# Kernel optimization log

Hardware: AMD Instinct MI355X
Metric: run time of the kernel (lower is better)

The kernel has to match this reference:

```python
import jax, jax.numpy as jnp
import numpy as np
import math

IN_FEATURES = 4096
OUT_FEATURES = 4096
N_ROWS = 8192
EPS = 1e-6
ROOT2 = math.sqrt(2.0)


def setup_inputs() -> dict:
    key = jax.random.key(0)
    k1, k2 = jax.random.split(key)
    # p_x: probabilities in [0,1]
    p_x = jax.random.uniform(k1, (N_ROWS, IN_FEATURES), dtype=jnp.float32)
    # weight ~ Uniform(-2, 2) per reset_parameters
    weight = jax.random.uniform(k2, (OUT_FEATURES, IN_FEATURES), dtype=jnp.float32, minval=-2.0, maxval=2.0)
    return {"p_x": p_x, "weight": weight}


def reference(p_x, weight):
    in_features = weight.shape[1]
    threshold = -(-in_features // 2)  # ceil(in_features / 2)
    p_w = jax.nn.sigmoid(weight)  # (O, I)
    # p_success = 2*p_w*p_x + 1 - p_x - p_w = c*p_x + d, with:
    c = 2.0 * p_w - 1.0          # (O, I)
    d = 1.0 - p_w                # (O, I)
    # mu = sum_i p_success = p_x @ c^T + sum_i d   -- never materialize (..., O, I)
    mu = jnp.einsum('ni,oi->no', p_x, c) + jnp.sum(d, axis=-1)  # (N, O)
    # sum_i p_success^2 = p_x^2 @ (c^2)^T + 2 * p_x @ (c*d)^T + sum_i d^2
    sum_sq = (jnp.einsum('ni,oi->no', p_x * p_x, c * c)
              + 2.0 * jnp.einsum('ni,oi->no', p_x, c * d)
              + jnp.sum(d * d, axis=-1))  # (N, O)
    # sum p_success*(1 - p_success) = mu - sum_sq
    sigma = jnp.sqrt(mu - sum_sq + EPS)  # (N, O)
    p_actives = 0.5 - 0.5 * jax.lax.erf((threshold - 0.5 - mu) / (sigma * ROOT2))
    return p_actives
```

## Files before the change

kernel.cpp:

```cpp
#include <hip/hip_runtime.h>
#include <hip/hip_bf16.h>
#include <math.h>
#include <cstdint>

#define KDIM 4096
#define ODIM 4096
#define MDIM 8192
#define EPSF 1e-6f
#define TM05 2047.5f

typedef __bf16 bf16x8 __attribute__((ext_vector_type(8)));
typedef float f32x4 __attribute__((ext_vector_type(4)));
typedef unsigned short u16;

#define XY_DELTA (MDIM * KDIM)
#define CD_DELTA (ODIM * KDIM)

#define NITER (KDIM / 128)

__device__ __forceinline__ u16 f2bf(float f) {
  __hip_bfloat16 h = __float2bfloat16(f);
  return __builtin_bit_cast(u16, h);
}
__device__ __forceinline__ float bf2f(u16 b) {
  unsigned int u = ((unsigned int)b) << 16;
  return __builtin_bit_cast(float, u);
}

__device__ __forceinline__ void async_cp16(void* lds, const void* g) {
  __builtin_amdgcn_global_load_lds(
      (__attribute__((address_space(1))) void*)(uintptr_t)g,
      (__attribute__((address_space(3))) void*)lds, 16, 0, 0);
}

__global__ void prep_x_kernel(const float4* __restrict__ x4,
                              ushort4* __restrict__ Xb,
                              ushort4* __restrict__ Yb) {
  int i = blockIdx.x * blockDim.x + threadIdx.x;
  float4 v = x4[i];
  ushort4 xo, yo;
  xo.x = f2bf(v.x); xo.y = f2bf(v.y); xo.z = f2bf(v.z); xo.w = f2bf(v.w);
  yo.x = f2bf(v.x * (1.0f - v.x));
  yo.y = f2bf(v.y * (1.0f - v.y));
  yo.z = f2bf(v.z * (1.0f - v.z));
  yo.w = f2bf(v.w * (1.0f - v.w));
  Xb[i] = xo;
  Yb[i] = yo;
}

__device__ __forceinline__ void wcomp(float w, u16& cb, u16& c2b, float& sd, float& sde) {
  float pw = 1.0f / (1.0f + __expf(-w));
  float c  = 2.0f * pw - 1.0f;
  float d  = 1.0f - pw;
  cb  = f2bf(c);
  c2b = f2bf(c * c);
  sd  += d;
  sde += d * pw;
}

__global__ void prep_w_kernel(const float4* __restrict__ w4,
                              ushort4* __restrict__ Cb,
                              ushort4* __restrict__ C2b,
                              float* __restrict__ sumd,
                              float* __restrict__ sumde) {
  const int o = blockIdx.x;
  const int t = threadIdx.x;
  const float4* wr = w4 + (size_t)o * (KDIM / 4);
  ushort4* cr  = Cb  + (size_t)o * (KDIM / 4);
  ushort4* c2r = C2b + (size_t)o * (KDIM / 4);
  float sd = 0.f, sde = 0.f;
#pragma unroll
  for (int it = 0; it < KDIM / 4 / 256; ++it) {
    int k4 = t + it * 256;
    float4 w = wr[k4];
    ushort4 co, c2o;
    wcomp(w.x, co.x, c2o.x, sd, sde);
    wcomp(w.y, co.y, c2o.y, sd, sde);
    wcomp(w.z, co.z, c2o.z, sd, sde);
    wcomp(w.w, co.w, c2o.w, sd, sde);
    cr[k4]  = co;
    c2r[k4] = c2o;
  }
#pragma unroll
  for (int off = 32; off > 0; off >>= 1) {
    sd  += __shfl_down(sd, off);
    sde += __shfl_down(sde, off);
  }
  __shared__ float red[8];
  if ((t & 63) == 0) { red[t >> 6] = sd; red[4 + (t >> 6)] = sde; }
  __syncthreads();
  if (t == 0) {
    sumd[o]  = red[0] + red[1] + red[2] + red[3];
    sumde[o] = red[4] + red[5] + red[6] + red[7];
  }
}


#define STG2(bb, isB, half, src, koff) do {                                    \
    char* _d = smem + (bb) * 65536 + (isB) * 32768 + (half) * 16384 + tid * 16;\
    const u16* _s = (src) + (size_t)((half) * 128) * KDIM + (koff);            \
    async_cp16(_d, _s);                                                        \
    async_cp16(_d + 8192, _s + (size_t)64 * KDIM);                             \
  } while (0)

#define BAR   asm volatile("s_barrier" ::: "memory")
#define BARV4 asm volatile("s_waitcnt vmcnt(4)\n\ts_barrier" ::: "memory")
#define BARV0 asm volatile("s_waitcnt vmcnt(0)\n\ts_barrier" ::: "memory")

#define PH(bb, AI, MO, GK, BARR, DOB, STG, ENDBAR) {                           \
    const char* Ab = smem + (bb) * 65536;                                      \
    const char* Bb = Ab + 32768;                                               \
    bf16x8 x0 = *(const bf16x8*)(Ab + arow + (MO) + 0 * 2048 + (GK));          \
    bf16x8 x1 = *(const bf16x8*)(Ab + arow + (MO) + 1 * 2048 + (GK));          \
    bf16x8 x2 = *(const bf16x8*)(Ab + arow + (MO) + 2 * 2048 + (GK));          \
    bf16x8 x3 = *(const bf16x8*)(Ab + arow + (MO) + 3 * 2048 + (GK));          \
    if (DOB) {                                                                 \
      _Pragma("unroll") for (int j = 0; j < 4; ++j)                            \
        BARR[j] = *(const bf16x8*)(Bb + brow + j * 2048 + (GK));               \
    }                                                                          \
    STG;                                                                       \
    asm volatile("s_waitcnt lgkmcnt(0)" ::: "memory");                         \
    __builtin_amdgcn_sched_barrier(0);                                         \
    __builtin_amdgcn_s_setprio(1);                                             \
    _Pragma("unroll") for (int j = 0; j < 4; ++j)                              \
      acc[(AI) + 0][j] = __builtin_amdgcn_mfma_f32_16x16x32_bf16(x0, BARR[j], acc[(AI) + 0][j], 0, 0, 0); \
    _Pragma("unroll") for (int j = 0; j < 4; ++j)                              \
      acc[(AI) + 1][j] = __builtin_amdgcn_mfma_f32_16x16x32_bf16(x1, BARR[j], acc[(AI) + 1][j], 0, 0, 0); \
    _Pragma("unroll") for (int j = 0; j < 4; ++j)                              \
      acc[(AI) + 2][j] = __builtin_amdgcn_mfma_f32_16x16x32_bf16(x2, BARR[j], acc[(AI) + 2][j], 0, 0, 0); \
    _Pragma("unroll") for (int j = 0; j < 4; ++j)                              \
      acc[(AI) + 3][j] = __builtin_amdgcn_mfma_f32_16x16x32_bf16(x3, BARR[j], acc[(AI) + 3][j], 0, 0, 0); \
    __builtin_amdgcn_s_setprio(0);                                             \
    ENDBAR;                                                                    \
  }

template <int PASS>
__global__ __launch_bounds__(512, 2) void gemm_pass_kernel(
    const u16* __restrict__ Ag, const u16* __restrict__ Bg,
    const float* __restrict__ sumd, const float* __restrict__ sumde,
    float* __restrict__ out) {
  __shared__ __attribute__((aligned(128))) char smem[2 * 65536];

  const int tid  = threadIdx.x;
  const int lane = tid & 63;
  const int wave = tid >> 6;
  const int wr   = wave >> 2;
  const int wc   = wave & 3;
  const int quad = lane >> 4;
  const int r16  = lane & 15;

  const int raw = blockIdx.x;
  const int wg  = (raw & 7) * 64 + (raw >> 3);
  const int n0  = (wg >> 5) * 256;
  const int m0  = (wg & 31) * 256;

  const int srow = tid >> 3;
  const int scol = ((tid & 7) ^ (srow & 7)) * 8;
  const u16* gA = Ag + (size_t)(m0 + srow) * KDIM + scol;
  const u16* gB = Bg + (size_t)(n0 + srow) * KDIM + scol;

  const int r7   = r16 & 7;
  const int g0   = (quad ^ r7) * 16;
  const int g1   = ((4 | quad) ^ r7) * 16;
  const int arow = (wr * 128 + r16) * 128;
  const int brow = (wc * 64 + r16) * 128;

  f32x4 acc[8][4];
#pragma unroll
  for (int i = 0; i < 8; ++i)
#pragma unroll
    for (int j = 0; j < 4; ++j) acc[i][j] = f32x4{0.f, 0.f, 0.f, 0.f};

  bf16x8 b0[4], b1[4];

  STG2(0, 0, 0, gA, 0); STG2(0, 0, 1, gA, 0);
  STG2(0, 1, 0, gB, 0); STG2(0, 1, 1, gB, 0);
  STG2(1, 1, 0, gB, 64); STG2(1, 1, 1, gB, 64);
  BARV4;

  for (int s = 0; s < NITER; ++s) {
    const bool nl = (s + 1 < NITER);
    PH(0, 0, 0,    g0, b0, 1, STG2(1, 0, 0, gA, 64), BAR)
    PH(0, 0, 0,    g1, b1, 1, STG2(1, 0, 1, gA, 64), BAR)
    PH(0, 4, 8192, g0, b0, 0, if (nl) STG2(0, 1, 0, gB, 128), BAR)
    PH(0, 4, 8192, g1, b1, 0, if (nl) STG2(0, 1, 1, gB, 128),
       if (nl) { BARV4; } else { BARV0; })
    PH(1, 0, 0,    g0, b0, 1, if (nl) STG2(0, 0, 0, gA, 128), BAR)
    PH(1, 0, 0,    g1, b1, 1, if (nl) STG2(0, 0, 1, gA, 128), BAR)
    PH(1, 4, 8192, g0, b0, 0, if (nl) STG2(1, 1, 0, gB, 192), BAR)
    PH(1, 4, 8192, g1, b1, 0, if (nl) STG2(1, 1, 1, gB, 192),
       if (nl) { BARV4; } else { BARV0; })
    gA += 128; gB += 128;
  }

  if (PASS == 0) {
#pragma unroll
    for (int j = 0; j < 4; ++j) {
      const int col = n0 + wc * 64 + j * 16 + r16;
#pragma unroll
      for (int i = 0; i < 8; ++i) {
        const int row = m0 + wr * 128 + i * 16 + quad * 4;
        f32x4 v = acc[i][j];
#pragma unroll
        for (int r = 0; r < 4; ++r) out[(size_t)(row + r) * ODIM + col] = v[r];
      }
    }
  } else {
    const float inv_rt2 = 0.70710678118654752f;
#pragma unroll
    for (int j = 0; j < 4; ++j) {
      const int col = n0 + wc * 64 + j * 16 + r16;
      const float sd  = sumd[col];
      const float sde = sumde[col] + EPSF;
#pragma unroll
      for (int i = 0; i < 8; ++i) {
        const int row = m0 + wr * 128 + i * 16 + quad * 4;
        f32x4 m4 = acc[i][j];
#pragma unroll
        for (int r = 0; r < 4; ++r) {
          float var = out[(size_t)(row + r) * ODIM + col] + sde;
          float mu  = m4[r] + sd;
          float z = (TM05 - mu) * rsqrtf(var) * inv_rt2;
          out[(size_t)(row + r) * ODIM + col] = 0.5f * erfcf(z);
        }
      }
    }
  }
}

extern "C" void kernel_launch(void* const* d_in, const int* in_sizes, int n_in,
                              void* d_out, int out_size, void* d_ws, size_t ws_size,
                              hipStream_t stream) {
  const float* p_x    = (const float*)d_in[0];
  const float* weight = (const float*)d_in[1];
  float* out = (float*)d_out;
  char* ws = (char*)d_ws;

  u16* Cb      = (u16*)(ws);
  u16* C2b     = (u16*)(ws + 33554432);
  float* sumd  = (float*)(ws + 67108864);
  float* sumde = (float*)(ws + 67125248);
  u16* Xb      = (u16*)(ws + 67141632);
  u16* Yb      = (u16*)(ws + 134250496);

  prep_w_kernel<<<ODIM, 256, 0, stream>>>((const float4*)weight, (ushort4*)Cb,
                                          (ushort4*)C2b, sumd, sumde);
  prep_x_kernel<<<(MDIM * KDIM / 4) / 256, 256, 0, stream>>>((const float4*)p_x,
                                                             (ushort4*)Xb,
                                                             (ushort4*)Yb);
  const int nwg = (MDIM / 256) * (ODIM / 256);
  gemm_pass_kernel<0><<<nwg, 512, 0, stream>>>(Yb, C2b, sumd, sumde, out);
  gemm_pass_kernel<1><<<nwg, 512, 0, stream>>>(Xb, Cb, sumd, sumde, out);
}
```

Baseline: 775.5 us.

## Software-pipeline LDS fragment loads one phase ahead of MFMA compute

Restructures the GEMM main loop so each phase issues the shared-memory reads for the next phase's A/B fragments while the MFMAs consume fragments loaded in the previous phase. It double-buffers the register fragments (ae/ao, b0/b1), uses partial lgkmcnt waits, and reorders the global-to-LDS stage schedule, dropping some barriers and loosening the vmcnt waits. The aim is to hide LDS latency behind matrix math. In exchange it uses more registers, and the barrier and buffer hazard reasoning becomes subtler, which risks reading data before it has arrived.

After: 776.3 us. Within noise of the previous version (+0.1%).

```diff
diff --git a/kernel.cpp b/kernel.cpp
--- a/kernel.cpp
+++ b/kernel.cpp
@@ -104,34 +104,34 @@
   } while (0)
 
 #define BAR   asm volatile("s_barrier" ::: "memory")
-#define BARV4 asm volatile("s_waitcnt vmcnt(4)\n\ts_barrier" ::: "memory")
+#define BARV2 asm volatile("s_waitcnt vmcnt(2)\n\ts_barrier" ::: "memory")
 #define BARV0 asm volatile("s_waitcnt vmcnt(0)\n\ts_barrier" ::: "memory")
 
-#define PH(bb, AI, MO, GK, BARR, DOB, STG, ENDBAR) {                           \
-    const char* Ab = smem + (bb) * 65536;                                      \
-    const char* Bb = Ab + 32768;                                               \
-    bf16x8 x0 = *(const bf16x8*)(Ab + arow + (MO) + 0 * 2048 + (GK));          \
-    bf16x8 x1 = *(const bf16x8*)(Ab + arow + (MO) + 1 * 2048 + (GK));          \
-    bf16x8 x2 = *(const bf16x8*)(Ab + arow + (MO) + 2 * 2048 + (GK));          \
-    bf16x8 x3 = *(const bf16x8*)(Ab + arow + (MO) + 3 * 2048 + (GK));          \
+#define PH(RBB, RMO, RGK, RA, DOB, RB, UA, UB, AI, STG, WN, ENDB) {            \
+    const char* Ab_ = smem + (RBB) * 65536;                                    \
+    const char* Bb_ = Ab_ + 32768;                                             \
+    RA[0] = *(const bf16x8*)(Ab_ + arow + (RMO) + 0 * 2048 + (RGK));           \
+    RA[1] = *(const bf16x8*)(Ab_ + arow + (RMO) + 1 * 2048 + (RGK));           \
+    RA[2] = *(const bf16x8*)(Ab_ + arow + (RMO) + 2 * 2048 + (RGK));           \
+    RA[3] = *(const bf16x8*)(Ab_ + arow + (RMO) + 3 * 2048 + (RGK));           \
     if (DOB) {                                                                 \
       _Pragma("unroll") for (int j = 0; j < 4; ++j)                            \
-        BARR[j] = *(const bf16x8*)(Bb + brow + j * 2048 + (GK));               \
+        RB[j] = *(const bf16x8*)(Bb_ + brow + j * 2048 + (RGK));               \
     }                                                                          \
     STG;                                                                       \
-    asm volatile("s_waitcnt lgkmcnt(0)" ::: "memory");                         \
+    asm volatile("s_waitcnt lgkmcnt(" #WN ")" ::: "memory");                   \
     __builtin_amdgcn_sched_barrier(0);                                         \
     __builtin_amdgcn_s_setprio(1);                                             \
     _Pragma("unroll") for (int j = 0; j < 4; ++j)                              \
-      acc[(AI) + 0][j] = __builtin_amdgcn_mfma_f32_16x16x32_bf16(x0, BARR[j], acc[(AI) + 0][j], 0, 0, 0); \
-    _Pragma("unroll") for (int j = 0; j < 4; ++j)                              \
-      acc[(AI) + 1][j] = __builtin_amdgcn_mfma_f32_16x16x32_bf16(x1, BARR[j], acc[(AI) + 1][j], 0, 0, 0); \
-    _Pragma("unroll") for (int j = 0; j < 4; ++j)                              \
-      acc[(AI) + 2][j] = __builtin_amdgcn_mfma_f32_16x16x32_bf16(x2, BARR[j], acc[(AI) + 2][j], 0, 0, 0); \
-    _Pragma("unroll") for (int j = 0; j < 4; ++j)                              \
-      acc[(AI) + 3][j] = __builtin_amdgcn_mfma_f32_16x16x32_bf16(x3, BARR[j], acc[(AI) + 3][j], 0, 0, 0); \
+      acc[(AI) + 0][j] = __builtin_amdgcn_mfma_f32_16x16x32_bf16(UA[0], UB[j], acc[(AI) + 0][j], 0, 0, 0); \
+    _Pragma("unroll") for (int j = 0; j < 4; ++j)                              \
+      acc[(AI) + 1][j] = __builtin_amdgcn_mfma_f32_16x16x32_bf16(UA[1], UB[j], acc[(AI) + 1][j], 0, 0, 0); \
+    _Pragma("unroll") for (int j = 0; j < 4; ++j)                              \
+      acc[(AI) + 2][j] = __builtin_amdgcn_mfma_f32_16x16x32_bf16(UA[2], UB[j], acc[(AI) + 2][j], 0, 0, 0); \
+    _Pragma("unroll") for (int j = 0; j < 4; ++j)                              \
+      acc[(AI) + 3][j] = __builtin_amdgcn_mfma_f32_16x16x32_bf16(UA[3], UB[j], acc[(AI) + 3][j], 0, 0, 0); \
     __builtin_amdgcn_s_setprio(0);                                             \
-    ENDBAR;                                                                    \
+    ENDB;                                                                      \
   }
 
 template <int PASS>
@@ -171,25 +171,32 @@
 #pragma unroll
     for (int j = 0; j < 4; ++j) acc[i][j] = f32x4{0.f, 0.f, 0.f, 0.f};
 
-  bf16x8 b0[4], b1[4];
+  bf16x8 ae[4], ao[4], b0[4], b1[4];
 
   STG2(0, 0, 0, gA, 0); STG2(0, 0, 1, gA, 0);
   STG2(0, 1, 0, gB, 0); STG2(0, 1, 1, gB, 0);
   STG2(1, 1, 0, gB, 64); STG2(1, 1, 1, gB, 64);
-  BARV4;
+  asm volatile("s_waitcnt vmcnt(4)\n\ts_barrier" ::: "memory");
+
+#pragma unroll
+  for (int i = 0; i < 4; ++i)
+    ae[i] = *(const bf16x8*)(smem + arow + i * 2048 + g0);
+#pragma unroll
+  for (int j = 0; j < 4; ++j)
+    b0[j] = *(const bf16x8*)(smem + 32768 + brow + j * 2048 + g0);
 
   for (int s = 0; s < NITER; ++s) {
     const bool nl = (s + 1 < NITER);
-    PH(0, 0, 0,    g0, b0, 1, STG2(1, 0, 0, gA, 64), BAR)
-    PH(0, 0, 0,    g1, b1, 1, STG2(1, 0, 1, gA, 64), BAR)
-    PH(0, 4, 8192, g0, b0, 0, if (nl) STG2(0, 1, 0, gB, 128), BAR)
-    PH(0, 4, 8192, g1, b1, 0, if (nl) STG2(0, 1, 1, gB, 128),
-       if (nl) { BARV4; } else { BARV0; })
-    PH(1, 0, 0,    g0, b0, 1, if (nl) STG2(0, 0, 0, gA, 128), BAR)
-    PH(1, 0, 0,    g1, b1, 1, if (nl) STG2(0, 0, 1, gA, 128), BAR)
-    PH(1, 4, 8192, g0, b0, 0, if (nl) STG2(1, 1, 0, gB, 192), BAR)
-    PH(1, 4, 8192, g1, b1, 0, if (nl) STG2(1, 1, 1, gB, 192),
-       if (nl) { BARV4; } else { BARV0; })
+    PH(0, 0,    g1, ao, 1, b1, ae, b0, 0, STG2(1, 0, 0, gA, 64), 8, )
+    PH(0, 8192, g0, ae, 0, b0, ao, b1, 0, STG2(1, 0, 1, gA, 64), 4, BAR)
+    PH(0, 8192, g1, ao, 0, b0, ae, b0, 4, if (nl) STG2(0, 1, 0, gB, 128), 4,
+       if (nl) { BARV2; } else { BARV0; })
+    PH(1, 0,    g0, ae, 1, b0, ao, b1, 4, if (nl) STG2(0, 1, 1, gB, 128), 8, BAR)
+    PH(1, 0,    g1, ao, 1, b1, ae, b0, 0, if (nl) STG2(0, 0, 0, gA, 128), 8, )
+    PH(1, 8192, g0, ae, 0, b0, ao, b1, 0, if (nl) STG2(0, 0, 1, gA, 128), 4, BAR)
+    PH(1, 8192, g1, ao, 0, b0, ae, b0, 4, if (nl) STG2(1, 1, 0, gB, 192), 4,
+       if (nl) { BARV2; } else { BARV0; })
+    PH(0, 0,    g0, ae, 1, b0, ao, b1, 4, if (nl) STG2(1, 1, 1, gB, 192), 8, BAR)
     gA += 128; gB += 128;
   }
 
```
